# Kernel tuning notes

Measured on AMD Instinct MI355X. Metric: run time of the kernel, lower is better.

The kernel has to match this reference:

```python
import jax, jax.numpy as jnp
import numpy as np

B, T_PH, H = 32, 512, 256
N_BINS = 256
DUR_MAX = 8
MAX_LEN = T_PH * DUR_MAX  # 4096


def setup_inputs() -> dict:
    key = jax.random.key(0)
    k = jax.random.split(key, 6)
    x = jax.random.normal(k[0], (B, T_PH, H), dtype=jnp.float32)
    pitch_target = jax.random.normal(k[1], (B, T_PH), dtype=jnp.float32)
    energy_target = jax.random.normal(k[2], (B, T_PH), dtype=jnp.float32)
    duration = jax.random.randint(k[3], (B, T_PH), 0, DUR_MAX).astype(jnp.int32)
    # sorted bin boundaries (linear quantization, as in pitch_quantization='linear')
    pitch_bins = jnp.linspace(-3.0, 3.0, N_BINS - 1, dtype=jnp.float32)
    energy_bins = jnp.linspace(-3.0, 3.0, N_BINS - 1, dtype=jnp.float32)
    pitch_emb = jax.random.normal(k[4], (N_BINS, H), dtype=jnp.float32) * 0.02
    energy_emb = jax.random.normal(k[5], (N_BINS, H), dtype=jnp.float32) * 0.02
    return {
        "x": x,
        "pitch_target": pitch_target,
        "energy_target": energy_target,
        "pitch_bins": pitch_bins,
        "energy_bins": energy_bins,
        "pitch_emb": pitch_emb,
        "energy_emb": energy_emb,
        "duration": duration,
        "max_len": MAX_LEN,
    }


def reference(x, pitch_target, energy_target, pitch_bins, energy_bins,
              pitch_emb, energy_emb, duration, max_len):
    # --- phoneme-level pitch/energy: bucketize + embedding lookup, add to x ---
    # torch.bucketize(v, bins) (right=False) == searchsorted(bins, v, side='left')
    p_idx = jnp.searchsorted(pitch_bins, pitch_target)      # [B, T_ph] int
    x = x + pitch_emb[p_idx]                                 # gather [B, T_ph, H]
    e_idx = jnp.searchsorted(energy_bins, energy_target)
    x = x + energy_emb[e_idx]

    # --- LengthRegulator: expand phoneme i duration[b,i] times, pad to max_len ---
    dur = duration.astype(jnp.int32)
    csum = jnp.cumsum(dur, axis=1)                           # [B, T_ph]
    mel_len = csum[:, -1]                                    # [B]
    t = jnp.arange(max_len, dtype=jnp.int32)                 # [M]
    # frame t belongs to phoneme idx where csum[idx-1] <= t < csum[idx]
    ph_idx = jax.vmap(lambda c: jnp.searchsorted(c, t, side='right'))(csum)  # [B, M]
    ph_idx = jnp.minimum(ph_idx, dur.shape[1] - 1)
    out = jnp.take_along_axis(x, ph_idx[:, :, None], axis=1)  # [B, M, H]
    valid = (t[None, :] < mel_len[:, None])                   # [B, M] (padding)
    out = jnp.where(valid[:, :, None], out, 0.0)
    return out, mel_len
```

## Files before the change

kernel.cpp:

```cpp
#include <hip/hip_runtime.h>

#define B_SZ 32
#define T_PH 512
#define H_DIM 256
#define N_EDGES 255
#define MAX_LEN 4096
#define FPB 16

typedef float f32x4 __attribute__((ext_vector_type(4)));

__global__ void prep_kernel(const int* __restrict__ dur,
                            const float* __restrict__ pt,
                            const float* __restrict__ et,
                            const float* __restrict__ pbins,
                            const float* __restrict__ ebins,
                            int* __restrict__ frames,
                            float* __restrict__ mel_out) {
    const int b = blockIdx.x;
    const int tid = threadIdx.x;
    const int wave = tid >> 6;
    const int lane = tid & 63;
    __shared__ int cs[T_PH];
    __shared__ int packv[T_PH];
    __shared__ int wsum[8];
    __shared__ float pb[N_EDGES];
    __shared__ float eb[N_EDGES];

    if (tid < N_EDGES) pb[tid] = pbins[tid];
    else if (tid >= 256 && tid < 256 + N_EDGES) eb[tid - 256] = ebins[tid - 256];

    const int d = dur[b * T_PH + tid];
    int v = d;
#pragma unroll
    for (int off = 1; off < 64; off <<= 1) {
        int u = __shfl_up(v, off, 64);
        if (lane >= off) v += u;
    }
    if (lane == 63) wsum[wave] = v;
    __syncthreads();
    int woff = 0;
#pragma unroll
    for (int w = 0; w < 8; ++w) woff += (w < wave) ? wsum[w] : 0;
    v += woff;
    cs[tid] = v;

    const float pv = pt[b * T_PH + tid];
    const float ev = et[b * T_PH + tid];
    int lo = 0, hi = N_EDGES;
    while (lo < hi) { int m = (lo + hi) >> 1; if (pb[m] < pv) lo = m + 1; else hi = m; }
    const int pi = lo;
    lo = 0; hi = N_EDGES;
    while (lo < hi) { int m = (lo + hi) >> 1; if (eb[m] < ev) lo = m + 1; else hi = m; }
    const int ei = lo;
    packv[tid] = tid | (pi << 9) | (ei << 17);
    __syncthreads();

    const int mel = cs[T_PH - 1];

    const int t0 = tid * 8;
    int p = 0;
    if (t0 < mel) {
        int l = 0, h = T_PH;
        while (l < h) { int m = (l + h) >> 1; if (cs[m] > t0) h = m; else l = m + 1; }
        p = l;
    }
    int o[8];
#pragma unroll
    for (int j = 0; j < 8; ++j) {
        const int t = t0 + j;
        int vv = -1;
        if (t < mel) {
            while (cs[p] <= t) ++p;
            vv = packv[p];
        }
        o[j] = vv;
    }
    int4* fr = (int4*)(frames + (size_t)b * MAX_LEN);
    fr[tid * 2]     = make_int4(o[0], o[1], o[2], o[3]);
    fr[tid * 2 + 1] = make_int4(o[4], o[5], o[6], o[7]);

    if (tid == T_PH - 1) mel_out[b] = (float)mel;
}

__global__ void expand_kernel(const float* __restrict__ x,
                              const float* __restrict__ pemb,
                              const float* __restrict__ eemb,
                              const int* __restrict__ frames,
                              float* __restrict__ out) {
    const int wave  = threadIdx.x >> 6;
    const int lane4 = threadIdx.x & 63;
    const int base  = blockIdx.x * FPB;

    int pk[4];
#pragma unroll
    for (int j = 0; j < 4; ++j)
        pk[j] = frames[base + j * 4 + wave];

    f32x4 val[4];
#pragma unroll
    for (int j = 0; j < 4; ++j) {
        const int k = pk[j];
        f32x4 r = {0.f, 0.f, 0.f, 0.f};
        if (k >= 0) {
            const int frame = base + j * 4 + wave;
            const int b  = frame >> 12;
            const int ph = k & 511;
            const int pi = (k >> 9) & 255;
            const int ei = (k >> 17) & 255;
            const f32x4 a = ((const f32x4*)(x    + (size_t)(b * T_PH + ph) * H_DIM))[lane4];
            const f32x4 p = ((const f32x4*)(pemb + (size_t)pi * H_DIM))[lane4];
            const f32x4 e = ((const f32x4*)(eemb + (size_t)ei * H_DIM))[lane4];
            r = a + p + e;
        }
        val[j] = r;
    }
#pragma unroll
    for (int j = 0; j < 4; ++j) {
        const int frame = base + j * 4 + wave;
        __builtin_nontemporal_store(val[j], (f32x4*)out + (size_t)frame * 64 + lane4);
    }
}

extern "C" void kernel_launch(void* const* d_in, const int* in_sizes, int n_in,
                              void* d_out, int out_size, void* d_ws, size_t ws_size,
                              hipStream_t stream) {
    const float* x     = (const float*)d_in[0];
    const float* pt    = (const float*)d_in[1];
    const float* et    = (const float*)d_in[2];
    const float* pbins = (const float*)d_in[3];
    const float* ebins = (const float*)d_in[4];
    const float* pemb  = (const float*)d_in[5];
    const float* eemb  = (const float*)d_in[6];
    const int*   dur   = (const int*)d_in[7];

    float* out = (float*)d_out;
    float* mel_out = out + (size_t)B_SZ * MAX_LEN * H_DIM;

    int* frames = (int*)d_ws;

    prep_kernel<<<B_SZ, T_PH, 0, stream>>>(dur, pt, et, pbins, ebins,
                                           frames, mel_out);

    const int nframes = B_SZ * MAX_LEN;
    expand_kernel<<<nframes / FPB, 256, 0, stream>>>(x, pemb, eemb, frames, out);
}
```

Baseline: 34.92 us.

## Process 64 frames per block with XCD-aware block remap and branchless loads

The expand kernel now launches 2048 blocks that each handle 64 frames instead of 16. Block indices are remapped so that consecutive virtual blocks land on the same XCD (phys&7 chunking), which is meant to improve L2 reuse of the x rows for a batch. Loads are now unconditional using index 0 for padding frames, with a select to zero afterwards. This removes divergence and lets more loads stay in flight per wave, at the cost of extra loads for padded frames and higher register pressure from 16 outstanding iterations.

```diff
diff --git a/kernel.cpp b/kernel.cpp
--- a/kernel.cpp
+++ b/kernel.cpp
@@ -5,7 +5,7 @@
 #define H_DIM 256
 #define N_EDGES 255
 #define MAX_LEN 4096
-#define FPB 16
+#define EXP_BLOCKS 2048
 
 typedef float f32x4 __attribute__((ext_vector_type(4)));
 
@@ -89,35 +89,32 @@
                               float* __restrict__ out) {
     const int wave  = threadIdx.x >> 6;
     const int lane4 = threadIdx.x & 63;
-    const int base  = blockIdx.x * FPB;
+    const int phys = blockIdx.x;
+    const int vb   = (phys & 7) * (EXP_BLOCKS / 8) + (phys >> 3);
+    const int fbase = vb * 64;
+    const int b = fbase >> 12;
+    const float* __restrict__ xb = x + (size_t)b * T_PH * H_DIM;
 
-    int pk[4];
+    int pks[16];
 #pragma unroll
-    for (int j = 0; j < 4; ++j)
-        pk[j] = frames[base + j * 4 + wave];
+    for (int i = 0; i < 16; ++i)
+        pks[i] = frames[fbase + i * 4 + wave];
 
-    f32x4 val[4];
 #pragma unroll
-    for (int j = 0; j < 4; ++j) {
-        const int k = pk[j];
-        f32x4 r = {0.f, 0.f, 0.f, 0.f};
-        if (k >= 0) {
-            const int frame = base + j * 4 + wave;
-            const int b  = frame >> 12;
-            const int ph = k & 511;
-            const int pi = (k >> 9) & 255;
-            const int ei = (k >> 17) & 255;
-            const f32x4 a = ((const f32x4*)(x    + (size_t)(b * T_PH + ph) * H_DIM))[lane4];
-            const f32x4 p = ((const f32x4*)(pemb + (size_t)pi * H_DIM))[lane4];
-            const f32x4 e = ((const f32x4*)(eemb + (size_t)ei * H_DIM))[lane4];
-            r = a + p + e;
-        }
-        val[j] = r;
-    }
-#pragma unroll
-    for (int j = 0; j < 4; ++j) {
-        const int frame = base + j * 4 + wave;
-        __builtin_nontemporal_store(val[j], (f32x4*)out + (size_t)frame * 64 + lane4);
+    for (int i = 0; i < 16; ++i) {
+        const int k  = pks[i];
+        const int kk = k >= 0 ? k : 0;
+        const int ph = kk & 511;
+        const int pi = (kk >> 9) & 255;
+        const int ei = (kk >> 17) & 255;
+        const f32x4 a = ((const f32x4*)(xb   + (size_t)ph * H_DIM))[lane4];
+        const f32x4 p = ((const f32x4*)(pemb + (size_t)pi * H_DIM))[lane4];
+        const f32x4 e = ((const f32x4*)(eemb + (size_t)ei * H_DIM))[lane4];
+        f32x4 r = a + p + e;
+        const f32x4 z = {0.f, 0.f, 0.f, 0.f};
+        r = (k >= 0) ? r : z;
+        const int frame = fbase + i * 4 + wave;
+        __builtin_nontemporal_store(r, (f32x4*)out + (size_t)frame * 64 + lane4);
     }
 }
 
@@ -141,6 +138,5 @@
     prep_kernel<<<B_SZ, T_PH, 0, stream>>>(dur, pt, et, pbins, ebins,
                                            frames, mel_out);
 
-    const int nframes = B_SZ * MAX_LEN;
-    expand_kernel<<<nframes / FPB, 256, 0, stream>>>(x, pemb, eemb, frames, out);
+    expand_kernel<<<EXP_BLOCKS, 256, 0, stream>>>(x, pemb, eemb, frames, out);
 }
```

After: 37.34 us. 1.07x slower.
